# Kernel tuning notes

Hardware: AMD Instinct MI355X
Metric: run time of the kernel (lower is better)

The kernel has to match this reference:

```python
import jax, jax.numpy as jnp
import numpy as np

B, NA, NB, E = 2, 256, 256, 512
H1, H2 = 300, 100


def setup_inputs() -> dict:
    key = jax.random.key(0)
    ks = jax.random.split(key, 16)

    def n(k, shape, scale=1.0):
        return jax.random.normal(k, shape, dtype=jnp.float32) * scale

    z = lambda shape: jnp.zeros(shape, jnp.float32)
    return {
        "action_embedding": n(ks[0], (B, E, NA)),
        "anchor_embedding": n(ks[1], (B, E, NB)),
        "action_points": n(ks[2], (B, 3, NA)),
        "anchor_points": n(ks[3], (B, 3, NB)),
        # pairwise MLP kernel params: 2E -> 300 -> 100 -> 1
        "mlp_W1": n(ks[4], (2 * E, H1), (2 * E) ** -0.5),
        "mlp_b1": z((H1,)),
        "mlp_W2": n(ks[5], (H1, H2), H1 ** -0.5),
        "mlp_b2": z((H2,)),
        "mlp_W3": n(ks[6], (H2, 1), H2 ** -0.5),
        "mlp_b3": z((1,)),
        # PointNet [512,64,64,64,128,512] (1x1 convs) + Conv1d(512,1,bias=False)
        "pn_W0": n(ks[7], (64, 512), 512 ** -0.5),
        "pn_b0": z((64,)),
        "pn_W1": n(ks[8], (64, 64), 64 ** -0.5),
        "pn_b1": z((64,)),
        "pn_W2": n(ks[9], (64, 64), 64 ** -0.5),
        "pn_b2": z((64,)),
        "pn_W3": n(ks[10], (128, 64), 64 ** -0.5),
        "pn_b3": z((128,)),
        "pn_W4": n(ks[11], (512, 128), 128 ** -0.5),
        "pn_b4": z((512,)),
        "head_W": n(ks[12], (1, 512), 512 ** -0.5),
    }


def reference(action_embedding, anchor_embedding, action_points, anchor_points,
              mlp_W1, mlp_b1, mlp_W2, mlp_b2, mlp_W3, mlp_b3,
              pn_W0, pn_b0, pn_W1, pn_b1, pn_W2, pn_b2, pn_W3, pn_b3,
              pn_W4, pn_b4, head_W):
    P_A = action_points.transpose(0, 2, 1)      # (B, NA, 3)
    P_B = anchor_points.transpose(0, 2, 1)      # (B, NB, 3)
    Phi_A = action_embedding.transpose(0, 2, 1)  # (B, NA, E)
    Phi_B = anchor_embedding.transpose(0, 2, 1)  # (B, NB, E)
    Ed = Phi_A.shape[-1]

    # --- symmetric pairwise MLP kernel: softplus((mlp(cat(a,b)) + mlp(cat(b,a))) / 2) ---
    # First Linear layer is split so the O(NA*NB*2E) concat is never materialized:
    # cat(a,b) @ W1 == a @ W1[:E] + b @ W1[E:]
    W1a, W1b = mlp_W1[:Ed], mlp_W1[Ed:]

    def mlp_tail(h):  # h: (B, NA, NB, H1) pre-activation of layer 1
        h = jax.nn.relu(h)
        h = jax.nn.relu(h @ mlp_W2 + mlp_b2)
        return (h @ mlp_W3 + mlp_b3)[..., 0]  # (B, NA, NB)

    hA_a = Phi_A @ W1a  # (B, NA, H1)
    hA_b = Phi_A @ W1b
    hB_a = Phi_B @ W1a  # (B, NB, H1)
    hB_b = Phi_B @ W1b
    v1 = mlp_tail(hA_a[:, :, None, :] + hB_b[:, None, :, :] + mlp_b1)  # mlp(cat(x1,x2))
    v2 = mlp_tail(hB_a[:, None, :, :] + hA_b[:, :, None, :] + mlp_b1)  # mlp(cat(x2,x1))
    R_est = jax.nn.softplus((v1 + v2) * 0.5)  # (B, NA, NB) estimated distances

    # --- weighted multilateration (estimate_p), vectorized over (B, NA) ---
    # Linearized LS: ||p||^2 - 2 q_k^T p = r_k^2 - ||q_k||^2; subtract weighted means
    # to eliminate ||p||^2, then solve 3x3 weighted normal equations per action point.
    w = jnp.ones(P_B.shape[:2], R_est.dtype)            # (B, NB) uniform weights (last_attn=False)
    wsum = w.sum(-1, keepdims=True)                      # (B, 1)
    qbar = (w[..., None] * P_B).sum(1) / wsum            # (B, 3)
    bvec = (P_B ** 2).sum(-1)[:, None, :] - R_est ** 2   # (B, NA, NB)
    bbar = (w[:, None, :] * bvec).sum(-1) / wsum         # (B, NA)
    Amat = 2.0 * (P_B - qbar[:, None, :])                # (B, NB, 3)
    yvec = bvec - bbar[..., None]                        # (B, NA, NB)
    M = jnp.einsum('bki,bk,bkj->bij', Amat, w, Amat)     # (B, 3, 3)
    rhs = jnp.einsum('bki,bk,bak->bai', Amat, w, yvec)   # (B, NA, 3)
    P_A_B_pred = jnp.linalg.solve(M[:, None], rhs[..., None])[..., 0]  # (B, NA, 3)

    flow = (P_A_B_pred - P_A).transpose(0, 2, 1)         # (B, 3, NA)

    # --- PointNet flow-weight head (1x1 convs + ReLU, final conv no bias) ---
    x = action_embedding                                  # (B, 512, NA)
    for Wc, bc in ((pn_W0, pn_b0), (pn_W1, pn_b1), (pn_W2, pn_b2),
                   (pn_W3, pn_b3), (pn_W4, pn_b4)):
        x = jax.nn.relu(jnp.einsum('oi,bin->bon', Wc, x) + bc[None, :, None])
    weight = jnp.einsum('oi,bin->bon', head_W, x)        # (B, 1, NA)

    full_flow = jnp.concatenate([flow, weight], axis=1)  # (B, 4, NA)
    return full_flow
```

## Files before the change

### kernel.cpp

```cpp
#include <hip/hip_runtime.h>
#include <hip/hip_bf16.h>
#include <hip/hip_fp16.h>

typedef float f32x4 __attribute__((ext_vector_type(4)));
typedef short s16x8 __attribute__((ext_vector_type(8)));
typedef _Float16 f16x8 __attribute__((ext_vector_type(8)));

#define OFF_EMBT   0u
#define OFF_W1T    1048576u
#define OFF_W2TSW  1662976u
#define OFF_W0BF   1734656u
#define OFF_HA     1800192u
#define OFF_R2     3110912u
#define WS_TOTAL   3635200u

__device__ __forceinline__ int pack_bf2(float a, float b) {
  __hip_bfloat162 h = __float22bfloat162_rn(make_float2(a, b));
  int r; __builtin_memcpy(&r, &h, 4); return r;
}
__device__ __forceinline__ unsigned pack_f16_2(float a, float b) {
  __half2 h = __float22half2_rn(make_float2(a, b));
  unsigned r; __builtin_memcpy(&r, &h, 4); return r;
}
__device__ __forceinline__ unsigned short bf16u(float f) {
  __hip_bfloat16 h = __float2bfloat16(f);
  unsigned short u; __builtin_memcpy(&u, &h, 2); return u;
}
__device__ __forceinline__ s16x8 i4_to_s8(int a, int b, int c, int d) {
  union { int i[4]; s16x8 s; } u;
  u.i[0] = a; u.i[1] = b; u.i[2] = c; u.i[3] = d; return u.s;
}

__global__ __launch_bounds__(256) void ka_prep(
    const float* __restrict__ act_emb, const float* __restrict__ anc_emb,
    const float* __restrict__ W1, const float* __restrict__ W2,
    const float* __restrict__ W0pn, char* __restrict__ ws)
{
  __hip_bfloat16* embT  = (__hip_bfloat16*)(ws + OFF_EMBT);
  __hip_bfloat16* W1T   = (__hip_bfloat16*)(ws + OFF_W1T);
  unsigned short* W2Tsw = (unsigned short*)(ws + OFF_W2TSW);
  unsigned short* W0bf  = (unsigned short*)(ws + OFF_W0BF);
  __shared__ float tile[64][65];
  int blk = blockIdx.x, t = threadIdx.x;
  if (blk < 128) {
    int b = blk >> 6, emb = (blk >> 5) & 1, ntile = (blk >> 3) & 3, etile = blk & 7;
    const float* src = emb ? anc_emb : act_emb;
    int e0 = etile * 64, n0 = ntile * 64;
    int rr = t >> 6, cc = t & 63;
    #pragma unroll
    for (int it2 = 0; it2 < 16; ++it2) {
      int e_l = rr * 16 + it2;
      tile[e_l][cc] = src[(size_t)(b * 512 + e0 + e_l) * 256 + n0 + cc];
    }
    __syncthreads();
    int n_l = t >> 2, eq = t & 3;
    unsigned int* dst = (unsigned int*)(embT + ((size_t)((b * 2 + emb) * 256 + n0 + n_l)) * 512 + e0 + eq * 16);
    #pragma unroll
    for (int kk = 0; kk < 8; ++kk)
      dst[kk] = (unsigned)pack_bf2(tile[eq * 16 + 2 * kk][n_l], tile[eq * 16 + 2 * kk + 1][n_l]);
  } else if (blk < 208) {
    int id = blk - 128;
    int half = id / 40; int rem = id % 40; int et = rem / 5; int ct = rem % 5;
    int e0 = et * 64, c0 = ct * 64;
    int rr = t >> 6, cc = t & 63;
    #pragma unroll
    for (int it2 = 0; it2 < 16; ++it2) {
      int e_l = rr * 16 + it2;
      int c = c0 + cc;
      tile[e_l][cc] = (c < 300) ? W1[(size_t)(half * 512 + e0 + e_l) * 300 + c] : 0.f;
    }
    __syncthreads();
    int c_l = t >> 2, eq = t & 3;
    if (c0 + c_l < 300) {
      unsigned int* dst = (unsigned int*)(W1T + ((size_t)(half * 300 + c0 + c_l)) * 512 + e0 + eq * 16);
      #pragma unroll
      for (int kk = 0; kk < 8; ++kk)
        dst[kk] = (unsigned)pack_bf2(tile[eq * 16 + 2 * kk][c_l], tile[eq * 16 + 2 * kk + 1][c_l]);
    }
  } else if (blk < 226) {
    int idx = (blk - 208) * 256 + t;
    if (idx < 4480) {
      int nt = idx / 640; int rem = idx - nt * 640; int ks = rem >> 6; int lane = rem & 63;
      int n = nt * 16 + (lane & 15);
      int kb = ks * 32 + (lane >> 4) * 8;
      unsigned int q[4];
      #pragma unroll
      for (int jj = 0; jj < 4; ++jj) {
        int k0 = kb + jj * 2, k1 = kb + jj * 2 + 1;
        float f0 = (n < 100 && k0 < 300) ? W2[(size_t)k0 * 100 + n] : 0.f;
        float f1 = (n < 100 && k1 < 300) ? W2[(size_t)k1 * 100 + n] : 0.f;
        q[jj] = pack_f16_2(f0, f1);
      }
      ((uint4*)W2Tsw)[idx] = make_uint4(q[0], q[1], q[2], q[3]);
    }
  } else if (blk < 242) {
    int idx = (blk - 226) * 256 + t;
    const float* s = W0pn + (size_t)idx * 8;
    ((uint4*)W0bf)[idx] = make_uint4(
        (unsigned)pack_bf2(s[0], s[1]), (unsigned)pack_bf2(s[2], s[3]),
        (unsigned)pack_bf2(s[4], s[5]), (unsigned)pack_bf2(s[6], s[7]));
  } else {
    int idx = (blk - 242) * 256 + t;
    _Float16* ha = (_Float16*)(ws + OFF_HA);
    #pragma unroll
    for (int rr = 0; rr < 2; ++rr) {
      int row = idx * 2 + rr;
      unsigned* p = (unsigned*)(ha + (size_t)row * 320 + 300);
      #pragma unroll
      for (int q2 = 0; q2 < 10; ++q2) p[q2] = 0u;
    }
  }
}

template<int K, int NT>
__device__ __forceinline__ void pn_layer(unsigned short* xb, const float* __restrict__ W,
                                         const float* __restrict__ bias, int wv, int l, int g)
{
  constexpr int NN = NT / 4;
  f32x4 z = {0.f, 0.f, 0.f, 0.f};
  f32x4 acc[NN];
  #pragma unroll
  for (int nn = 0; nn < NN; ++nn) acc[nn] = z;
  #pragma unroll
  for (int nn = 0; nn < NN; ++nn) {
    int o = (wv + nn * 4) * 16 + l;
    const float* wr0 = W + (size_t)o * K;
    #pragma unroll
    for (int ks = 0; ks < K / 32; ++ks) {
      int koff = ks * 32 + g * 8;
      f32x4 wa = *(const f32x4*)(wr0 + koff);
      f32x4 wb = *(const f32x4*)(wr0 + koff + 4);
      s16x8 bfr = i4_to_s8(pack_bf2(wa.x, wa.y), pack_bf2(wa.z, wa.w),
                           pack_bf2(wb.x, wb.y), pack_bf2(wb.z, wb.w));
      s16x8 a0 = *(const s16x8*)(xb + (size_t)l * 520 + koff);
      acc[nn] = __builtin_amdgcn_mfma_f32_16x16x32_bf16(a0, bfr, acc[nn], 0, 0, 0);
    }
  }
  __syncthreads();
  #pragma unroll
  for (int nn = 0; nn < NN; ++nn) {
    int chan = (wv + nn * 4) * 16 + l;
    float bv = bias[chan];
    #pragma unroll
    for (int r = 0; r < 4; ++r)
      xb[(size_t)(g * 4 + r) * 520 + chan] = bf16u(fmaxf(acc[nn][r] + bv, 0.f));
  }
  __syncthreads();
}

__global__ __launch_bounds__(256) void k1_ha(
    const __hip_bfloat16* __restrict__ embT, const __hip_bfloat16* __restrict__ W1T,
    const float* __restrict__ b1, _Float16* __restrict__ ha_ws,
    const unsigned short* __restrict__ W0bf,
    const float* __restrict__ pnW1, const float* __restrict__ pnW2,
    const float* __restrict__ pnW3, const float* __restrict__ pnW4,
    const float* __restrict__ pnB0, const float* __restrict__ pnB1,
    const float* __restrict__ pnB2, const float* __restrict__ pnB3,
    const float* __restrict__ pnB4,
    const float* __restrict__ headW, float* __restrict__ out)
{
  __shared__ unsigned short xbuf[16 * 520];
  int blk = blockIdx.x, t = threadIdx.x;
  int wv = t >> 6, lane = t & 63, l = lane & 15, g = lane >> 4;
  if (blk < 320) {
    int b = blk / 160; int r = blk % 160; int emb = r / 80; r %= 80;
    int mch = r / 5; int nch = r % 5;
    int m0 = mch * 16;
    const unsigned short* Ap = (const unsigned short*)embT +
        ((size_t)((b * 2 + emb) * 256 + m0 + l)) * 512;
    const unsigned short* Wp = (const unsigned short*)W1T;
    f32x4 z = {0.f, 0.f, 0.f, 0.f};
    f32x4 acc[2] = {z, z};
    for (int ks = 0; ks < 16; ++ks) {
      int k0 = ks * 32 + g * 8;
      s16x8 af = *(const s16x8*)(Ap + k0);
      #pragma unroll
      for (int q = 0; q < 2; ++q) {
        int c = nch * 120 + (wv * 2 + q) * 16 + l;
        s16x8 bf = {0, 0, 0, 0, 0, 0, 0, 0};
        if (c < 600) bf = *(const s16x8*)(Wp + (size_t)c * 512 + k0);
        acc[q] = __builtin_amdgcn_mfma_f32_16x16x32_bf16(af, bf, acc[q], 0, 0, 0);
      }
    }
    #pragma unroll
    for (int q = 0; q < 2; ++q) {
      int cl = (wv * 2 + q) * 16 + l;
      int c = nch * 120 + cl;
      if (cl < 120 && c < 600) {
        int half = (c >= 300) ? 1 : 0;
        int cc = c - half * 300;
        float bias = (emb == 0) ? b1[cc] : 0.f;
        _Float16* Dp = ha_ws + ((size_t)((b * 4 + emb * 2 + half) * 256 + m0 + g * 4)) * 320 + cc;
        #pragma unroll
        for (int r2 = 0; r2 < 4; ++r2)
          Dp[(size_t)r2 * 320] = (_Float16)__float2half_rn(acc[q][r2] + bias);
      }
    }
  } else {
    int pn = blk - 320;
    int b_pn = pn >> 4, n0 = (pn & 15) * 16;
    unsigned short* xb = xbuf;
    {
      const unsigned short* A0 = (const unsigned short*)embT + ((size_t)(b_pn * 2 * 256 + n0)) * 512;
      f32x4 acc0 = {0.f, 0.f, 0.f, 0.f};
      int o = wv * 16 + l;
      const unsigned short* w0r = W0bf + (size_t)o * 512;
      #pragma unroll
      for (int ks = 0; ks < 16; ++ks) {
        int koff = ks * 32 + g * 8;
        s16x8 bfr = *(const s16x8*)(w0r + koff);
        s16x8 a0 = *(const s16x8*)(A0 + (size_t)l * 512 + koff);
        acc0 = __builtin_amdgcn_mfma_f32_16x16x32_bf16(a0, bfr, acc0, 0, 0, 0);
      }
      float bv = pnB0[o];
      #pragma unroll
      for (int r2 = 0; r2 < 4; ++r2)
        xb[(size_t)(g * 4 + r2) * 520 + o] = bf16u(fmaxf(acc0[r2] + bv, 0.f));
      __syncthreads();
    }
    pn_layer<64, 4>(xb, pnW1, pnB1, wv, l, g);
    pn_layer<64, 4>(xb, pnW2, pnB2, wv, l, g);
    pn_layer<64, 8>(xb, pnW3, pnB3, wv, l, g);
    pn_layer<128, 32>(xb, pnW4, pnB4, wv, l, g);
    {
      int p_l = t >> 4, os = t & 15;
      const unsigned short* row = xb + (size_t)p_l * 520 + os * 32;
      float s = 0.f;
      #pragma unroll
      for (int c = 0; c < 32; ++c) {
        unsigned int u = ((unsigned int)row[c]) << 16;
        float xv; __builtin_memcpy(&xv, &u, 4);
        s += xv * headW[os * 32 + c];
      }
      s += __shfl_xor(s, 1); s += __shfl_xor(s, 2);
      s += __shfl_xor(s, 4); s += __shfl_xor(s, 8);
      if (os == 0) out[(size_t)(b_pn * 4 + 3) * 256 + n0 + p_l] = s;
    }
  }
}

__global__ __launch_bounds__(512, 4) void k2_main(
    const _Float16* __restrict__ ha_ws, const unsigned short* __restrict__ W2Tsw,
    const float* __restrict__ b2g, const float* __restrict__ W3g, const float* __restrict__ b3g,
    float* __restrict__ R2)
{
  __shared__ int4 w2s[4480];
  int blk = blockIdx.x, t = threadIdx.x;
  int wv = t >> 6, lane = t & 63, l = lane & 15, g = lane >> 4;
  int b = blk >> 9, it = (blk >> 5) & 15, jt = blk & 31;
  int i0 = it * 16, j = jt * 8 + wv;
  {
    const int4* w2g = (const int4*)W2Tsw;
    for (int u = t; u < 4480; u += 512) w2s[u] = w2g[u];
  }
  const _Float16* hap0 = ha_ws + ((size_t)((b * 4 + 0) * 256 + i0 + l)) * 320 + g * 8;
  const _Float16* hap1 = ha_ws + ((size_t)((b * 4 + 1) * 256 + i0 + l)) * 320 + g * 8;
  const _Float16* hbp0 = ha_ws + ((size_t)((b * 4 + 3) * 256 + j)) * 320 + g * 8;
  const _Float16* hbp1 = ha_ws + ((size_t)((b * 4 + 2) * 256 + j)) * 320 + g * 8;
  f16x8 ha0c = *(const f16x8*)(hap0);
  f16x8 ha1c = *(const f16x8*)(hap1);
  f16x8 hb0c = *(const f16x8*)(hbp0);
  f16x8 hb1c = *(const f16x8*)(hbp1);
  __syncthreads();
  f32x4 z = {0.f, 0.f, 0.f, 0.f};
  f32x4 acc0[7], acc1[7];
  #pragma unroll
  for (int nt = 0; nt < 7; ++nt) { acc0[nt] = z; acc1[nt] = z; }
  const f16x8 zf = {0, 0, 0, 0, 0, 0, 0, 0};
  #pragma unroll 1
  for (int ks = 0; ks < 10; ++ks) {
    f16x8 ha0n, ha1n, hb0n, hb1n;
    if (ks < 9) {
      int noff = (ks + 1) * 32;
      ha0n = *(const f16x8*)(hap0 + noff);
      ha1n = *(const f16x8*)(hap1 + noff);
      hb0n = *(const f16x8*)(hbp0 + noff);
      hb1n = *(const f16x8*)(hbp1 + noff);
    }
    f16x8 af0 = __builtin_elementwise_max(ha0c + hb0c, zf);
    f16x8 af1 = __builtin_elementwise_max(ha1c + hb1c, zf);
    const int4* wp = &w2s[ks * 64 + lane];
    #pragma unroll
    for (int nt = 0; nt < 7; ++nt) {
      f16x8 bf = *(const f16x8*)(wp + nt * 640);
      acc0[nt] = __builtin_amdgcn_mfma_f32_16x16x32_f16(af0, bf, acc0[nt], 0, 0, 0);
      acc1[nt] = __builtin_amdgcn_mfma_f32_16x16x32_f16(af1, bf, acc1[nt], 0, 0, 0);
    }
    ha0c = ha0n; ha1c = ha1n; hb0c = hb0n; hb1c = hb1n;
  }
  {
    float w3v[7], b2v[7];
    #pragma unroll
    for (int nt = 0; nt < 7; ++nt) {
      int n = nt * 16 + l;
      w3v[nt] = (n < 100) ? W3g[n] : 0.f;
      b2v[nt] = (n < 100) ? b2g[n] : 0.f;
    }
    float b3 = b3g[0];
    #pragma unroll
    for (int r = 0; r < 4; ++r) {
      float pv = 0.f;
      #pragma unroll
      for (int nt = 0; nt < 7; ++nt) {
        pv += fmaxf(acc0[nt][r] + b2v[nt], 0.f) * w3v[nt];
        pv += fmaxf(acc1[nt][r] + b2v[nt], 0.f) * w3v[nt];
      }
      pv += __shfl_xor(pv, 1);
      pv += __shfl_xor(pv, 2);
      pv += __shfl_xor(pv, 4);
      pv += __shfl_xor(pv, 8);
      float S = 0.5f * pv + b3;
      float Rr = (S > 20.f) ? S : log1pf(expf(S));
      if (l == 0)
        R2[((size_t)(b * 256 + i0 + g * 4 + r)) * 256 + j] = Rr * Rr;
    }
  }
}

__device__ __forceinline__ float block_sum(float v, float* redbuf, int t) {
  #pragma unroll
  for (int m = 1; m < 64; m <<= 1) v += __shfl_xor(v, m);
  __syncthreads();
  if ((t & 63) == 0) redbuf[t >> 6] = v;
  __syncthreads();
  return redbuf[0] + redbuf[1] + redbuf[2] + redbuf[3];
}

__global__ __launch_bounds__(256) void k3_solve(
    const float* __restrict__ anc_pts, const float* __restrict__ act_pts,
    const float* __restrict__ R2, float* __restrict__ out)
{
  __shared__ float Ax[256], Ay[256], Az[256];
  __shared__ float redbuf[4];
  int blk = blockIdx.x, t = threadIdx.x;
  int b = blk >> 2, ic = blk & 3;
  int k = t;
  float px = anc_pts[(size_t)(b * 3 + 0) * 256 + k];
  float py = anc_pts[(size_t)(b * 3 + 1) * 256 + k];
  float pz = anc_pts[(size_t)(b * 3 + 2) * 256 + k];
  float qx = block_sum(px, redbuf, t) * (1.f / 256.f);
  float qy = block_sum(py, redbuf, t) * (1.f / 256.f);
  float qz = block_sum(pz, redbuf, t) * (1.f / 256.f);
  float ax = 2.f * (px - qx), ay = 2.f * (py - qy), az = 2.f * (pz - qz);
  float p2 = px * px + py * py + pz * pz;
  Ax[k] = ax; Ay[k] = ay; Az[k] = az;
  float mxx = block_sum(ax * ax, redbuf, t);
  float mxy = block_sum(ax * ay, redbuf, t);
  float mxz = block_sum(ax * az, redbuf, t);
  float myy = block_sum(ay * ay, redbuf, t);
  float myz = block_sum(ay * az, redbuf, t);
  float mzz = block_sum(az * az, redbuf, t);
  float c0x = block_sum(ax * p2, redbuf, t);
  float c0y = block_sum(ay * p2, redbuf, t);
  float c0z = block_sum(az * p2, redbuf, t);
  __syncthreads();
  float det = mxx * (myy * mzz - myz * myz) - mxy * (mxy * mzz - myz * mxz) + mxz * (mxy * myz - myy * mxz);
  float idet = 1.f / det;
  float i00 = (myy * mzz - myz * myz) * idet;
  float i01 = (mxz * myz - mxy * mzz) * idet;
  float i02 = (mxy * myz - mxz * myy) * idet;
  float i11 = (mxx * mzz - mxz * mxz) * idet;
  float i12 = (mxy * mxz - mxx * myz) * idet;
  float i22 = (mxx * myy - mxy * mxy) * idet;
  int il = t >> 2, ks = t & 3;
  int i = ic * 64 + il;
  const float* rrow = R2 + ((size_t)(b * 256 + i)) * 256;
  float r0 = 0.f, r1 = 0.f, r2 = 0.f;
  #pragma unroll
  for (int kk = 0; kk < 16; ++kk) {
    int kb = ks * 64 + kk * 4;
    f32x4 rv = *(const f32x4*)(rrow + kb);
    r0 += Ax[kb] * rv.x + Ax[kb + 1] * rv.y + Ax[kb + 2] * rv.z + Ax[kb + 3] * rv.w;
    r1 += Ay[kb] * rv.x + Ay[kb + 1] * rv.y + Ay[kb + 2] * rv.z + Ay[kb + 3] * rv.w;
    r2 += Az[kb] * rv.x + Az[kb + 1] * rv.y + Az[kb + 2] * rv.z + Az[kb + 3] * rv.w;
  }
  r0 += __shfl_xor(r0, 1); r0 += __shfl_xor(r0, 2);
  r1 += __shfl_xor(r1, 1); r1 += __shfl_xor(r1, 2);
  r2 += __shfl_xor(r2, 1); r2 += __shfl_xor(r2, 2);
  if (ks == 0) {
    float hx = c0x - r0, hy = c0y - r1, hz = c0z - r2;
    float x0 = i00 * hx + i01 * hy + i02 * hz;
    float x1 = i01 * hx + i11 * hy + i12 * hz;
    float x2 = i02 * hx + i12 * hy + i22 * hz;
    out[(size_t)(b * 4 + 0) * 256 + i] = x0 - act_pts[(size_t)(b * 3 + 0) * 256 + i];
    out[(size_t)(b * 4 + 1) * 256 + i] = x1 - act_pts[(size_t)(b * 3 + 1) * 256 + i];
    out[(size_t)(b * 4 + 2) * 256 + i] = x2 - act_pts[(size_t)(b * 3 + 2) * 256 + i];
  }
}

extern "C" void kernel_launch(void* const* d_in, const int* in_sizes, int n_in,
                              void* d_out, int out_size, void* d_ws, size_t ws_size,
                              hipStream_t stream)
{
  const float* act_emb = (const float*)d_in[0];
  const float* anc_emb = (const float*)d_in[1];
  const float* act_pts = (const float*)d_in[2];
  const float* anc_pts = (const float*)d_in[3];
  const float* W1  = (const float*)d_in[4];
  const float* b1  = (const float*)d_in[5];
  const float* W2  = (const float*)d_in[6];
  const float* b2  = (const float*)d_in[7];
  const float* W3  = (const float*)d_in[8];
  const float* b3  = (const float*)d_in[9];
  const float* pnW0 = (const float*)d_in[10];
  const float* pnB0 = (const float*)d_in[11];
  const float* pnW1 = (const float*)d_in[12];
  const float* pnB1 = (const float*)d_in[13];
  const float* pnW2 = (const float*)d_in[14];
  const float* pnB2 = (const float*)d_in[15];
  const float* pnW3 = (const float*)d_in[16];
  const float* pnB3 = (const float*)d_in[17];
  const float* pnW4 = (const float*)d_in[18];
  const float* pnB4 = (const float*)d_in[19];
  const float* headW = (const float*)d_in[20];
  char* ws = (char*)d_ws;
  __hip_bfloat16* embT  = (__hip_bfloat16*)(ws + OFF_EMBT);
  __hip_bfloat16* W1T   = (__hip_bfloat16*)(ws + OFF_W1T);
  unsigned short* W2Tsw = (unsigned short*)(ws + OFF_W2TSW);
  unsigned short* W0bf  = (unsigned short*)(ws + OFF_W0BF);
  _Float16* ha_ws = (_Float16*)(ws + OFF_HA);
  float* R2ws  = (float*)(ws + OFF_R2);
  float* outp  = (float*)d_out;

  ka_prep<<<246, 256, 0, stream>>>(act_emb, anc_emb, W1, W2, pnW0, ws);
  k1_ha<<<352, 256, 0, stream>>>(embT, W1T, b1, ha_ws, W0bf,
                                 pnW1, pnW2, pnW3, pnW4, pnB0, pnB1, pnB2, pnB3, pnB4,
                                 headW, outp);
  k2_main<<<1024, 512, 0, stream>>>(ha_ws, W2Tsw, b2, W3, b3, R2ws);
  k3_solve<<<8, 256, 0, stream>>>(anc_pts, act_pts, R2ws, outp);
}
```

Measured before the change: 165.9 us.

## Switch pairwise MLP layer-2 to 32x32x16 MFMA with larger tiles

Rewrites the k2_main pairwise kernel to use 32x32x16 f16 MFMA instead of 16x16x32. Each block now covers 32 action rows and two j columns per wave, with the 100 output channels split across wave halves. The hidden-row stride shrinks from 320 to 304 and the W2 swizzled layout is rebuilt to match, which cuts padded K work from 320 to 304. The final reduction uses DPP and swizzle instead of shuffles plus an LDS exchange between wave halves. The grid is halved, trading more registers per thread (64 accumulators) and extra block syncs for higher MFMA efficiency and fewer redundant loads.

```diff
diff --git a/kernel.cpp b/kernel.cpp
--- a/kernel.cpp
+++ b/kernel.cpp
@@ -3,16 +3,17 @@
 #include <hip/hip_fp16.h>
 
 typedef float f32x4 __attribute__((ext_vector_type(4)));
+typedef float f32x16 __attribute__((ext_vector_type(16)));
 typedef short s16x8 __attribute__((ext_vector_type(8)));
 typedef _Float16 f16x8 __attribute__((ext_vector_type(8)));
 
 #define OFF_EMBT   0u
 #define OFF_W1T    1048576u
 #define OFF_W2TSW  1662976u
-#define OFF_W0BF   1734656u
-#define OFF_HA     1800192u
-#define OFF_R2     3110912u
-#define WS_TOTAL   3635200u
+#define OFF_W0BF   1740800u
+#define OFF_HA     1806336u
+#define OFF_R2     3051520u
+#define WS_TOTAL   3575808u
 
 __device__ __forceinline__ int pack_bf2(float a, float b) {
   __hip_bfloat162 h = __float22bfloat162_rn(make_float2(a, b));
@@ -29,6 +30,19 @@
 __device__ __forceinline__ s16x8 i4_to_s8(int a, int b, int c, int d) {
   union { int i[4]; s16x8 s; } u;
   u.i[0] = a; u.i[1] = b; u.i[2] = c; u.i[3] = d; return u.s;
+}
+template<int CTRL>
+__device__ __forceinline__ float dpp_add(float x) {
+  int xi; __builtin_memcpy(&xi, &x, 4);
+  int yi = __builtin_amdgcn_update_dpp(0, xi, CTRL, 0xf, 0xf, true);
+  float y; __builtin_memcpy(&y, &yi, 4);
+  return x + y;
+}
+__device__ __forceinline__ float swz_xor16(float x) {
+  int xi; __builtin_memcpy(&xi, &x, 4);
+  int yi = __builtin_amdgcn_ds_swizzle(xi, 0x401f);
+  float y; __builtin_memcpy(&y, &yi, 4);
+  return y;
 }
 
 __global__ __launch_bounds__(256) void ka_prep(
@@ -77,37 +91,34 @@
       for (int kk = 0; kk < 8; ++kk)
         dst[kk] = (unsigned)pack_bf2(tile[eq * 16 + 2 * kk][c_l], tile[eq * 16 + 2 * kk + 1][c_l]);
     }
-  } else if (blk < 226) {
+  } else if (blk < 227) {
     int idx = (blk - 208) * 256 + t;
-    if (idx < 4480) {
-      int nt = idx / 640; int rem = idx - nt * 640; int ks = rem >> 6; int lane = rem & 63;
-      int n = nt * 16 + (lane & 15);
-      int kb = ks * 32 + (lane >> 4) * 8;
-      unsigned int q[4];
-      #pragma unroll
-      for (int jj = 0; jj < 4; ++jj) {
-        int k0 = kb + jj * 2, k1 = kb + jj * 2 + 1;
-        float f0 = (n < 100 && k0 < 300) ? W2[(size_t)k0 * 100 + n] : 0.f;
-        float f1 = (n < 100 && k1 < 300) ? W2[(size_t)k1 * 100 + n] : 0.f;
-        q[jj] = pack_f16_2(f0, f1);
-      }
-      ((uint4*)W2Tsw)[idx] = make_uint4(q[0], q[1], q[2], q[3]);
-    }
-  } else if (blk < 242) {
-    int idx = (blk - 226) * 256 + t;
+    int lane = idx & 63; int ntks = idx >> 6; int nt = ntks & 3; int ks = ntks >> 2;
+    int n = nt * 32 + (lane & 31);
+    int kb = ks * 16 + (lane >> 5) * 8;
+    unsigned int q[4];
+    #pragma unroll
+    for (int jj = 0; jj < 4; ++jj) {
+      int k0 = kb + jj * 2, k1 = kb + jj * 2 + 1;
+      float f0 = (n < 100 && k0 < 300) ? W2[(size_t)k0 * 100 + n] : 0.f;
+      float f1 = (n < 100 && k1 < 300) ? W2[(size_t)k1 * 100 + n] : 0.f;
+      q[jj] = pack_f16_2(f0, f1);
+    }
+    ((uint4*)W2Tsw)[idx] = make_uint4(q[0], q[1], q[2], q[3]);
+  } else if (blk < 243) {
+    int idx = (blk - 227) * 256 + t;
     const float* s = W0pn + (size_t)idx * 8;
     ((uint4*)W0bf)[idx] = make_uint4(
         (unsigned)pack_bf2(s[0], s[1]), (unsigned)pack_bf2(s[2], s[3]),
         (unsigned)pack_bf2(s[4], s[5]), (unsigned)pack_bf2(s[6], s[7]));
   } else {
-    int idx = (blk - 242) * 256 + t;
+    int idx = (blk - 243) * 256 + t;
     _Float16* ha = (_Float16*)(ws + OFF_HA);
     #pragma unroll
     for (int rr = 0; rr < 2; ++rr) {
       int row = idx * 2 + rr;
-      unsigned* p = (unsigned*)(ha + (size_t)row * 320 + 300);
-      #pragma unroll
-      for (int q2 = 0; q2 < 10; ++q2) p[q2] = 0u;
+      unsigned* p = (unsigned*)(ha + (size_t)row * 304 + 300);
+      p[0] = 0u; p[1] = 0u;
     }
   }
 }
@@ -190,10 +201,10 @@
         int half = (c >= 300) ? 1 : 0;
         int cc = c - half * 300;
         float bias = (emb == 0) ? b1[cc] : 0.f;
-        _Float16* Dp = ha_ws + ((size_t)((b * 4 + emb * 2 + half) * 256 + m0 + g * 4)) * 320 + cc;
+        _Float16* Dp = ha_ws + ((size_t)((b * 4 + emb * 2 + half) * 256 + m0 + g * 4)) * 304 + cc;
         #pragma unroll
         for (int r2 = 0; r2 < 4; ++r2)
-          Dp[(size_t)r2 * 320] = (_Float16)__float2half_rn(acc[q][r2] + bias);
+          Dp[(size_t)r2 * 304] = (_Float16)__float2half_rn(acc[q][r2] + bias);
       }
     }
   } else {
@@ -244,75 +255,95 @@
     const float* __restrict__ b2g, const float* __restrict__ W3g, const float* __restrict__ b3g,
     float* __restrict__ R2)
 {
-  __shared__ int4 w2s[4480];
+  __shared__ int4 w2s[4864];
+  __shared__ float ex[4][2][16];
   int blk = blockIdx.x, t = threadIdx.x;
-  int wv = t >> 6, lane = t & 63, l = lane & 15, g = lane >> 4;
-  int b = blk >> 9, it = (blk >> 5) & 15, jt = blk & 31;
-  int i0 = it * 16, j = jt * 8 + wv;
+  int wv = t >> 6, lane = t & 63, col = lane & 31, hi = lane >> 5;
+  int jl = wv & 3, nh = wv >> 2;
+  int u = blk; int b = u >> 8; u &= 255; int it = u >> 5; int jtp = u & 31;
+  int i0 = it * 32;
+  int j0 = jtp * 8 + jl;
   {
     const int4* w2g = (const int4*)W2Tsw;
-    for (int u = t; u < 4480; u += 512) w2s[u] = w2g[u];
-  }
-  const _Float16* hap0 = ha_ws + ((size_t)((b * 4 + 0) * 256 + i0 + l)) * 320 + g * 8;
-  const _Float16* hap1 = ha_ws + ((size_t)((b * 4 + 1) * 256 + i0 + l)) * 320 + g * 8;
-  const _Float16* hbp0 = ha_ws + ((size_t)((b * 4 + 3) * 256 + j)) * 320 + g * 8;
-  const _Float16* hbp1 = ha_ws + ((size_t)((b * 4 + 2) * 256 + j)) * 320 + g * 8;
-  f16x8 ha0c = *(const f16x8*)(hap0);
-  f16x8 ha1c = *(const f16x8*)(hap1);
-  f16x8 hb0c = *(const f16x8*)(hbp0);
-  f16x8 hb1c = *(const f16x8*)(hbp1);
-  __syncthreads();
-  f32x4 z = {0.f, 0.f, 0.f, 0.f};
-  f32x4 acc0[7], acc1[7];
-  #pragma unroll
-  for (int nt = 0; nt < 7; ++nt) { acc0[nt] = z; acc1[nt] = z; }
+    #pragma unroll
+    for (int q = 0; q < 9; ++q) { int idx = t + q * 512; w2s[idx] = w2g[idx]; }
+    { int idx = t + 9 * 512; if (idx < 4864) w2s[idx] = w2g[idx]; }
+  }
+  const _Float16* pA0 = ha_ws + ((size_t)((b * 4 + 0) * 256 + i0 + col)) * 304 + hi * 8;
+  const _Float16* pA1 = ha_ws + ((size_t)((b * 4 + 1) * 256 + i0 + col)) * 304 + hi * 8;
+  const _Float16* pB0 = ha_ws + ((size_t)((b * 4 + 3) * 256 + j0)) * 304 + hi * 8;
+  const _Float16* pB1 = ha_ws + ((size_t)((b * 4 + 2) * 256 + j0)) * 304 + hi * 8;
+  f16x8 a0c = *(const f16x8*)(pA0);
+  f16x8 a1c = *(const f16x8*)(pA1);
+  f16x8 b0c = *(const f16x8*)(pB0);
+  f16x8 b1c = *(const f16x8*)(pB1);
+  __syncthreads();
+
   const f16x8 zf = {0, 0, 0, 0, 0, 0, 0, 0};
+  const int4* wbase = &w2s[nh * 128 + lane];
+  f32x16 z16;
+  #pragma unroll
+  for (int q = 0; q < 16; ++q) z16[q] = 0.f;
+
   #pragma unroll 1
-  for (int ks = 0; ks < 10; ++ks) {
-    f16x8 ha0n, ha1n, hb0n, hb1n;
-    if (ks < 9) {
-      int noff = (ks + 1) * 32;
-      ha0n = *(const f16x8*)(hap0 + noff);
-      ha1n = *(const f16x8*)(hap1 + noff);
-      hb0n = *(const f16x8*)(hbp0 + noff);
-      hb1n = *(const f16x8*)(hbp1 + noff);
-    }
-    f16x8 af0 = __builtin_elementwise_max(ha0c + hb0c, zf);
-    f16x8 af1 = __builtin_elementwise_max(ha1c + hb1c, zf);
-    const int4* wp = &w2s[ks * 64 + lane];
-    #pragma unroll
-    for (int nt = 0; nt < 7; ++nt) {
-      f16x8 bf = *(const f16x8*)(wp + nt * 640);
-      acc0[nt] = __builtin_amdgcn_mfma_f32_16x16x32_f16(af0, bf, acc0[nt], 0, 0, 0);
-      acc1[nt] = __builtin_amdgcn_mfma_f32_16x16x32_f16(af1, bf, acc1[nt], 0, 0, 0);
-    }
-    ha0c = ha0n; ha1c = ha1n; hb0c = hb0n; hb1c = hb1n;
-  }
-  {
-    float w3v[7], b2v[7];
-    #pragma unroll
-    for (int nt = 0; nt < 7; ++nt) {
-      int n = nt * 16 + l;
-      w3v[nt] = (n < 100) ? W3g[n] : 0.f;
-      b2v[nt] = (n < 100) ? b2g[n] : 0.f;
-    }
+  for (int s = 0; s < 2; ++s) {
+    f32x16 acc00 = z16, acc01 = z16, acc10 = z16, acc11 = z16;
+    #pragma unroll 1
+    for (int ks = 0; ks < 19; ++ks) {
+      f16x8 a0n, a1n, b0n, b1n;
+      if (ks < 18) {
+        int ko = (ks + 1) * 16;
+        a0n = *(const f16x8*)(pA0 + ko);
+        a1n = *(const f16x8*)(pA1 + ko);
+        b0n = *(const f16x8*)(pB0 + s * 1216 + ko);
+        b1n = *(const f16x8*)(pB1 + s * 1216 + ko);
+      } else if (s == 0) {
+        a0n = *(const f16x8*)(pA0);
+        a1n = *(const f16x8*)(pA1);
+        b0n = *(const f16x8*)(pB0 + 1216);
+        b1n = *(const f16x8*)(pB1 + 1216);
+      } else {
+        a0n = a0c; a1n = a1c; b0n = b0c; b1n = b1c;
+      }
+      f16x8 af0 = __builtin_elementwise_max(a0c + b0c, zf);
+      f16x8 af1 = __builtin_elementwise_max(a1c + b1c, zf);
+      const int4* wp = wbase + ks * 256;
+      f16x8 bf0 = *(const f16x8*)(wp);
+      f16x8 bf1 = *(const f16x8*)(wp + 64);
+      acc00 = __builtin_amdgcn_mfma_f32_32x32x16_f16(af0, bf0, acc00, 0, 0, 0);
+      acc01 = __builtin_amdgcn_mfma_f32_32x32x16_f16(af0, bf1, acc01, 0, 0, 0);
+      acc10 = __builtin_amdgcn_mfma_f32_32x32x16_f16(af1, bf0, acc10, 0, 0, 0);
+      acc11 = __builtin_amdgcn_mfma_f32_32x32x16_f16(af1, bf1, acc11, 0, 0, 0);
+      a0c = a0n; a1c = a1n; b0c = b0n; b1c = b1n;
+    }
+    int j = j0 + s * 4;
+    int n0 = nh * 64 + col, n1 = n0 + 32;
+    float w3v0 = (n0 < 100) ? W3g[n0] : 0.f;
+    float w3v1 = (n1 < 100) ? W3g[n1] : 0.f;
+    float b2v0 = (n0 < 100) ? b2g[n0] : 0.f;
+    float b2v1 = (n1 < 100) ? b2g[n1] : 0.f;
     float b3 = b3g[0];
-    #pragma unroll
-    for (int r = 0; r < 4; ++r) {
-      float pv = 0.f;
-      #pragma unroll
-      for (int nt = 0; nt < 7; ++nt) {
-        pv += fmaxf(acc0[nt][r] + b2v[nt], 0.f) * w3v[nt];
-        pv += fmaxf(acc1[nt][r] + b2v[nt], 0.f) * w3v[nt];
-      }
-      pv += __shfl_xor(pv, 1);
-      pv += __shfl_xor(pv, 2);
-      pv += __shfl_xor(pv, 4);
-      pv += __shfl_xor(pv, 8);
-      float S = 0.5f * pv + b3;
+    float mine = 0.f;
+    #pragma unroll
+    for (int r = 0; r < 16; ++r) {
+      float x = fmaxf(acc00[r] + b2v0, 0.f) * w3v0 + fmaxf(acc01[r] + b2v1, 0.f) * w3v1
+              + fmaxf(acc10[r] + b2v0, 0.f) * w3v0 + fmaxf(acc11[r] + b2v1, 0.f) * w3v1;
+      x = dpp_add<0xB1>(x);
+      x = dpp_add<0x4E>(x);
+      x = dpp_add<0x141>(x);
+      x = dpp_add<0x140>(x);
+      x += swz_xor16(x);
+      if (col == r) mine = x;
+    }
+    __syncthreads();
+    if (nh == 1 && col < 16) ex[jl][hi][col] = mine;
+    __syncthreads();
+    if (nh == 0 && col < 16) {
+      float tot = mine + ex[jl][hi][col];
+      float S = 0.5f * tot + b3;
       float Rr = (S > 20.f) ? S : log1pf(expf(S));
-      if (l == 0)
-        R2[((size_t)(b * 256 + i0 + g * 4 + r)) * 256 + j] = Rr * Rr;
+      int il = (col & 3) + 8 * (col >> 2) + 4 * hi;
+      R2[((size_t)(b * 256 + i0 + il)) * 256 + j] = Rr * Rr;
     }
   }
 }
@@ -422,10 +453,10 @@
   float* R2ws  = (float*)(ws + OFF_R2);
   float* outp  = (float*)d_out;
 
-  ka_prep<<<246, 256, 0, stream>>>(act_emb, anc_emb, W1, W2, pnW0, ws);
+  ka_prep<<<247, 256, 0, stream>>>(act_emb, anc_emb, W1, W2, pnW0, ws);
   k1_ha<<<352, 256, 0, stream>>>(embT, W1T, b1, ha_ws, W0bf,
                                  pnW1, pnW2, pnW3, pnW4, pnB0, pnB1, pnB2, pnB3, pnB4,
                                  headW, outp);
-  k2_main<<<1024, 512, 0, stream>>>(ha_ws, W2Tsw, b2, W3, b3, R2ws);
+  k2_main<<<512, 512, 0, stream>>>(ha_ws, W2Tsw, b2, W3, b3, R2ws);
   k3_solve<<<8, 256, 0, stream>>>(anc_pts, act_pts, R2ws, outp);
 }
```

Result: no change. 168.7 us (+1.7%).
